# Performance work log

Measured on AMD Instinct MI355X. Metric: run time of the kernel, lower is better.

Reference implementation:

```python
import jax, jax.numpy as jnp
import numpy as np

B, L, E, H = 8192, 64, 128, 8  # batch, max seq len, info_size, head_num
HD = E // H                    # head dim


def setup_inputs() -> dict:
    key = jax.random.key(0)
    k1, k2, k3, k4, k5, k6 = jax.random.split(key, 6)
    inter_info = jax.random.normal(k1, (B, L, E), dtype=jnp.float32)
    # ragged lengths in [1, L] (each sample has at least the query vector)
    lengths = jax.random.randint(k2, (B,), 1, L + 1, dtype=jnp.int32)
    s = 1.0 / np.sqrt(E)
    in_proj_w = jax.random.uniform(k3, (3 * E, E), dtype=jnp.float32, minval=-s, maxval=s)
    in_proj_b = jnp.zeros((3 * E,), dtype=jnp.float32)
    out_proj_w = jax.random.uniform(k4, (E, E), dtype=jnp.float32, minval=-s, maxval=s)
    out_proj_b = jnp.zeros((E,), dtype=jnp.float32)
    return {"inter_info": inter_info, "lengths": lengths,
            "in_proj_w": in_proj_w, "in_proj_b": in_proj_b,
            "out_proj_w": out_proj_w, "out_proj_b": out_proj_b}


def reference(inter_info, lengths, in_proj_w, in_proj_b, out_proj_w, out_proj_b):
    # Per sample: query = first vector, keys/values = all (valid) vectors.
    # Equivalent to torch nn.MultiheadAttention with 1 query per sample.
    Wq, Wk, Wv = in_proj_w[:E], in_proj_w[E:2 * E], in_proj_w[2 * E:]
    bq, bk, bv = in_proj_b[:E], in_proj_b[E:2 * E], in_proj_b[2 * E:]

    query_info = inter_info[:, 0]                                  # [B, E]
    q = (query_info @ Wq.T + bq).reshape(B, H, HD)                 # [B, H, hd]
    k = (inter_info @ Wk.T + bk).reshape(B, L, H, HD)              # [B, L, H, hd]
    v = (inter_info @ Wv.T + bv).reshape(B, L, H, HD)

    scores = jnp.einsum('bhd,blhd->bhl', q, k) / np.sqrt(HD)       # [B, H, L]
    valid = jnp.arange(L)[None, :] < lengths[:, None]              # [B, L]
    scores = jnp.where(valid[:, None, :], scores, -jnp.inf)
    attn = jax.nn.softmax(scores, axis=-1)                         # [B, H, L]

    ctx = jnp.einsum('bhl,blhd->bhd', attn, v).reshape(B, E)       # [B, E]
    attn_hidden = ctx @ out_proj_w.T + out_proj_b                  # [B, E]
    return attn_hidden, query_info
```

## Files before the change

### kernel.cpp

```cpp
#include <hip/hip_runtime.h>
#include <hip/hip_bf16.h>


typedef unsigned int  u32;
typedef unsigned short u16;

#define XR  136
#define XR4 17
#define YR  136
#define UR  136
#define SCR 68

typedef __attribute__((ext_vector_type(8))) __bf16 bf16x8;
typedef __attribute__((ext_vector_type(4))) float  f32x4;

struct __align__(16) Smem {
  u16   Xs[2][64 * XR];
  u16   u[2][8 * UR];
  u16   y[2][8 * YR];
  float q[2][128];
  float sc[2][8][SCR];
  float c[2][8];
  float ctx[2][128];
  int   isbf;
};

__device__ __forceinline__ float blo(u32 u) { return __uint_as_float(u << 16); }
__device__ __forceinline__ float bhi(u32 u) { return __uint_as_float(u & 0xffff0000u); }
__device__ __forceinline__ float b2f(u16 u) { return __uint_as_float(((u32)u) << 16); }
__device__ __forceinline__ u16 f2b(float f) {
  union { __hip_bfloat16 h; u16 u; } cv; cv.h = __float2bfloat16(f); return cv.u;
}
__device__ __forceinline__ u32 pack2(float a, float b) {
  return (u32)f2b(a) | ((u32)f2b(b) << 16);
}
__device__ __forceinline__ void unp8(uint4 v, float* o) {
  o[0]=blo(v.x); o[1]=bhi(v.x); o[2]=blo(v.y); o[3]=bhi(v.y);
  o[4]=blo(v.z); o[5]=bhi(v.z); o[6]=blo(v.w); o[7]=bhi(v.w);
}

template<bool BF>
__device__ __forceinline__ void load8(const void* p, size_t off, float* o) {
  if (BF) {
    unp8(*(const uint4*)((const u16*)p + off), o);
  } else {
    const float4* q4 = (const float4*)((const float*)p + off);
    float4 a = q4[0], b = q4[1];
    o[0]=a.x; o[1]=a.y; o[2]=a.z; o[3]=a.w;
    o[4]=b.x; o[5]=b.y; o[6]=b.z; o[7]=b.w;
  }
}
template<bool BF>
__device__ __forceinline__ void load4(const void* p, size_t off, float* o) {
  if (BF) {
    uint2 v = *(const uint2*)((const u16*)p + off);
    o[0]=blo(v.x); o[1]=bhi(v.x); o[2]=blo(v.y); o[3]=bhi(v.y);
  } else {
    float4 v = *(const float4*)((const float*)p + off);
    o[0]=v.x; o[1]=v.y; o[2]=v.z; o[3]=v.w;
  }
}
template<bool BF>
__device__ __forceinline__ float lds1(const void* p, size_t off) {
  return BF ? b2f(((const u16*)p)[off]) : ((const float*)p)[off];
}

template<bool BF>
__device__ __forceinline__ void body(Smem& S, int b0, int t,
    const void* inter, const int* lengths, const void* w_in, const void* b_in,
    const void* w_out, const void* b_out, void* out)
{
  const int len0 = lengths[b0];
  const int len1 = lengths[b0 + 1];

  if (BF) {
    const uint4* src = (const uint4*)inter + (size_t)b0 * 1024;
#pragma unroll
    for (int r = 0; r < 4; ++r) {
      int g = t + 512 * r;
      int tile = g >> 10, gg = g & 1023, l = gg >> 4, ci = gg & 15;
      if (l < (tile ? len1 : len0))
        ((uint4*)S.Xs[tile])[l * XR4 + ci] = src[g];
    }
  } else {
    const float4* src = (const float4*)inter + (size_t)b0 * 2048;
#pragma unroll
    for (int r = 0; r < 4; ++r) {
      int g = t + 512 * r;
      int tile = g >> 10, gg = g & 1023, l = gg >> 4, ci = gg & 15;
      if (l < (tile ? len1 : len0)) {
        float4 a = src[g * 2], b = src[g * 2 + 1];
        uint4 v;
        v.x = pack2(a.x, a.y); v.y = pack2(a.z, a.w);
        v.z = pack2(b.x, b.y); v.w = pack2(b.z, b.w);
        ((uint4*)S.Xs[tile])[l * XR4 + ci] = v;
      }
    }
  }
  __syncthreads();

  if (t < 128) {
    float a0 = 0.f, a1 = 0.f;
#pragma unroll
    for (int k = 0; k < 16; ++k) {
      float w8[8]; load8<BF>(w_in, (size_t)t * 128 + k * 8, w8);
      float xa[8]; unp8(((const uint4*)S.Xs[0])[k], xa);
      float xb[8]; unp8(((const uint4*)S.Xs[1])[k], xb);
#pragma unroll
      for (int j = 0; j < 8; ++j) {
        a0 = fmaf(w8[j], xa[j], a0);
        a1 = fmaf(w8[j], xb[j], a1);
      }
    }
    float bq = lds1<BF>(b_in, t);
    S.q[0][t] = a0 + bq;
    S.q[1][t] = a1 + bq;
  }
  __syncthreads();

  if (t < 256) {
    const int h = t >> 5, cc = t & 31;
    float a00=0.f,a01=0.f,a02=0.f,a03=0.f, a10=0.f,a11=0.f,a12=0.f,a13=0.f;
#pragma unroll
    for (int d = 0; d < 16; ++d) {
      float w4[4]; load4<BF>(w_in, (size_t)(128 + h * 16 + d) * 128 + cc * 4, w4);
      float q0 = S.q[0][h * 16 + d], q1 = S.q[1][h * 16 + d];
      a00 = fmaf(w4[0], q0, a00); a01 = fmaf(w4[1], q0, a01);
      a02 = fmaf(w4[2], q0, a02); a03 = fmaf(w4[3], q0, a03);
      a10 = fmaf(w4[0], q1, a10); a11 = fmaf(w4[1], q1, a11);
      a12 = fmaf(w4[2], q1, a12); a13 = fmaf(w4[3], q1, a13);
    }
    *(uint2*)&S.u[0][h * UR + cc * 4] = make_uint2(pack2(a00, a01), pack2(a02, a03));
    *(uint2*)&S.u[1][h * UR + cc * 4] = make_uint2(pack2(a10, a11), pack2(a12, a13));
    if (cc == 0) {
      float c0 = 0.f, c1 = 0.f;
      for (int d = 0; d < 16; ++d) {
        float bk = lds1<BF>(b_in, 128 + h * 16 + d);
        c0 += S.q[0][h * 16 + d] * bk;
        c1 += S.q[1][h * 16 + d] * bk;
      }
      S.c[0][h] = c0; S.c[1][h] = c1;
    }
  }
  __syncthreads();

  {
    const int w = t >> 6, lane = t & 63;
    const int bt = w >> 2, mt = w & 3;
    const int arow = mt * 16 + (lane & 15);
    const int col  = lane & 15;
    const int kb   = (lane >> 4) * 8;
    const bool hv  = (col < 8);
    f32x4 acc = {0.f, 0.f, 0.f, 0.f};
#pragma unroll
    for (int kc = 0; kc < 4; ++kc) {
      union { uint4 u4; bf16x8 b8; } a, b;
      a.u4 = *(const uint4*)&S.Xs[bt][arow * XR + kc * 32 + kb];
      b.u4 = *(const uint4*)&S.u[bt][(col & 7) * UR + kc * 32 + kb];
      if (!hv) b.u4 = make_uint4(0u, 0u, 0u, 0u);
      acc = __builtin_amdgcn_mfma_f32_16x16x32_bf16(a.b8, b.b8, acc, 0, 0, 0);
    }
    if (hv) {
      const int l0 = mt * 16 + (lane >> 4) * 4;
      const float cadd = S.c[bt][col];
      f32x4 o;
      o[0] = (acc[0] + cadd) * 0.25f;
      o[1] = (acc[1] + cadd) * 0.25f;
      o[2] = (acc[2] + cadd) * 0.25f;
      o[3] = (acc[3] + cadd) * 0.25f;
      *(f32x4*)&S.sc[bt][col][l0] = o;
    }
  }
  __syncthreads();

  {
    const int bt = t >> 8, h = (t >> 5) & 7, sub = t & 31;
    const int len = bt ? len1 : len0;
    const int l0 = sub, l1 = sub + 32;
    float s0 = S.sc[bt][h][l0], s1 = S.sc[bt][h][l1];
    const bool v0 = l0 < len, v1 = l1 < len;
    float m = fmaxf(v0 ? s0 : -INFINITY, v1 ? s1 : -INFINITY);
#pragma unroll
    for (int off = 16; off > 0; off >>= 1) m = fmaxf(m, __shfl_xor(m, off, 32));
    float e0 = v0 ? __expf(s0 - m) : 0.f;
    float e1 = v1 ? __expf(s1 - m) : 0.f;
    float s = e0 + e1;
#pragma unroll
    for (int off = 16; off > 0; off >>= 1) s += __shfl_xor(s, off, 32);
    float inv = 1.f / s;
    S.sc[bt][h][l0] = e0 * inv;
    S.sc[bt][h][l1] = e1 * inv;
  }
  __syncthreads();

  {
    const int bt = t >> 8, h = (t >> 5) & 7, cc = t & 31;
    const int len = bt ? len1 : len0;
    float a0 = 0.f, a1 = 0.f, a2 = 0.f, a3 = 0.f;
    const float* ar = S.sc[bt][h];
    const u16* xb = S.Xs[bt];
#pragma unroll 4
    for (int l = 0; l < len; ++l) {
      float av = ar[l];
      uint2 xv = *(const uint2*)&xb[l * XR + cc * 4];
      a0 = fmaf(av, blo(xv.x), a0); a1 = fmaf(av, bhi(xv.x), a1);
      a2 = fmaf(av, blo(xv.y), a2); a3 = fmaf(av, bhi(xv.y), a3);
    }
    *(uint2*)&S.y[bt][h * YR + cc * 4] = make_uint2(pack2(a0, a1), pack2(a2, a3));
  }
  __syncthreads();

  if (t < 128) {
    const int h = t >> 4;
    float a0 = 0.f, a1 = 0.f;
#pragma unroll
    for (int k = 0; k < 16; ++k) {
      float w8[8]; load8<BF>(w_in, (size_t)(256 + t) * 128 + k * 8, w8);
      float y0[8]; unp8(*(const uint4*)&S.y[0][h * YR + k * 8], y0);
      float y1[8]; unp8(*(const uint4*)&S.y[1][h * YR + k * 8], y1);
#pragma unroll
      for (int j = 0; j < 8; ++j) {
        a0 = fmaf(w8[j], y0[j], a0);
        a1 = fmaf(w8[j], y1[j], a1);
      }
    }
    float bv = lds1<BF>(b_in, 256 + t);
    S.ctx[0][t] = a0 + bv;
    S.ctx[1][t] = a1 + bv;
  }
  __syncthreads();

  if (t < 128) {
    float a0 = 0.f, a1 = 0.f;
#pragma unroll
    for (int k = 0; k < 16; ++k) {
      float w8[8]; load8<BF>(w_out, (size_t)t * 128 + k * 8, w8);
      float4 ca = *(const float4*)&S.ctx[0][k * 8];
      float4 cb = *(const float4*)&S.ctx[0][k * 8 + 4];
      float4 da = *(const float4*)&S.ctx[1][k * 8];
      float4 db = *(const float4*)&S.ctx[1][k * 8 + 4];
      a0 += w8[0]*ca.x + w8[1]*ca.y + w8[2]*ca.z + w8[3]*ca.w
          + w8[4]*cb.x + w8[5]*cb.y + w8[6]*cb.z + w8[7]*cb.w;
      a1 += w8[0]*da.x + w8[1]*da.y + w8[2]*da.z + w8[3]*da.w
          + w8[4]*db.x + w8[5]*db.y + w8[6]*db.z + w8[7]*db.w;
    }
    float bo = lds1<BF>(b_out, t);
    a0 += bo; a1 += bo;
    if (BF) {
      u16* o = (u16*)out;
      o[(size_t)b0 * 128 + t]       = f2b(a0);
      o[(size_t)(b0 + 1) * 128 + t] = f2b(a1);
    } else {
      float* o = (float*)out;
      o[(size_t)b0 * 128 + t]       = a0;
      o[(size_t)(b0 + 1) * 128 + t] = a1;
    }
  } else if (t >= 256) {
    const int tile = (t >> 7) & 1, e = t & 127;
    size_t o1 = (size_t)8192 * 128 + (size_t)(b0 + tile) * 128 + e;
    u16 xv = S.Xs[tile][e];
    if (BF) ((u16*)out)[o1] = xv;
    else    ((float*)out)[o1] = b2f(xv);
  }
}

__global__ __launch_bounds__(512, 6) void infoattn_kernel(
    const void* inter, const int* __restrict__ lengths,
    const void* w_in, const void* b_in, const void* w_out, const void* b_out,
    void* out)
{
  __shared__ Smem S;
  const int t = threadIdx.x;
  const int b0 = blockIdx.x * 2;

  if (t < 64) {
    float v = b2f(((const u16*)inter)[t]);
    bool bad = !(fabsf(v) < 1000.f);
    unsigned long long m = __ballot(bad);
    if (t == 0) S.isbf = (m == 0ull) ? 1 : 0;
  }
  __syncthreads();
  const bool isbf = (S.isbf != 0);

  if (isbf) body<true >(S, b0, t, inter, lengths, w_in, b_in, w_out, b_out, out);
  else      body<false>(S, b0, t, inter, lengths, w_in, b_in, w_out, b_out, out);
}

extern "C" void kernel_launch(void* const* d_in, const int* in_sizes, int n_in,
                              void* d_out, int out_size, void* d_ws, size_t ws_size,
                              hipStream_t stream) {
  infoattn_kernel<<<dim3(4096), dim3(512), 0, stream>>>(
      d_in[0], (const int*)d_in[1], d_in[2], d_in[3], d_in[4], d_in[5], d_out);
}
```

Measured before the change: 442.3 us.

## Spread small per-block GEMV stages across all 512 threads with split-K shuffles

The q projection, q·Wk fold, V projection and output projection stages previously ran on only 128 or 256 threads, each handling both batch tiles. They now use all 512 threads: each output element is split over two threads, each doing half of K, and the halves are combined with a lane xor-shuffle. The query passthrough write is handled by the idle half-threads. Launch bounds are also relaxed from 6 to 4 blocks per CU, which gives more registers per thread but may lower occupancy.

```diff
diff --git a/kernel.cpp b/kernel.cpp
--- a/kernel.cpp
+++ b/kernel.cpp
@@ -99,47 +99,39 @@
   }
   __syncthreads();
 
-  if (t < 128) {
-    float a0 = 0.f, a1 = 0.f;
-#pragma unroll
-    for (int k = 0; k < 16; ++k) {
-      float w8[8]; load8<BF>(w_in, (size_t)t * 128 + k * 8, w8);
-      float xa[8]; unp8(((const uint4*)S.Xs[0])[k], xa);
-      float xb[8]; unp8(((const uint4*)S.Xs[1])[k], xb);
-#pragma unroll
-      for (int j = 0; j < 8; ++j) {
-        a0 = fmaf(w8[j], xa[j], a0);
-        a1 = fmaf(w8[j], xb[j], a1);
-      }
-    }
-    float bq = lds1<BF>(b_in, t);
-    S.q[0][t] = a0 + bq;
-    S.q[1][t] = a1 + bq;
-  }
-  __syncthreads();
-
-  if (t < 256) {
-    const int h = t >> 5, cc = t & 31;
-    float a00=0.f,a01=0.f,a02=0.f,a03=0.f, a10=0.f,a11=0.f,a12=0.f,a13=0.f;
+  {
+    const int o = t >> 1, kh = t & 1;
+    const int bt = o >> 7, e = o & 127;
+    float a = 0.f;
+#pragma unroll
+    for (int k = 0; k < 8; ++k) {
+      const int kc = kh * 8 + k;
+      float w8[8]; load8<BF>(w_in, (size_t)e * 128 + kc * 8, w8);
+      float x8[8]; unp8(((const uint4*)S.Xs[bt])[kc], x8);
+#pragma unroll
+      for (int j = 0; j < 8; ++j) a = fmaf(w8[j], x8[j], a);
+    }
+    a += __shfl_xor(a, 1, 64);
+    if (kh == 0) S.q[bt][e] = a + lds1<BF>(b_in, e);
+  }
+  __syncthreads();
+
+  {
+    const int bt = t >> 8, h = (t >> 5) & 7, cc = t & 31;
+    float a0=0.f,a1=0.f,a2=0.f,a3=0.f;
 #pragma unroll
     for (int d = 0; d < 16; ++d) {
       float w4[4]; load4<BF>(w_in, (size_t)(128 + h * 16 + d) * 128 + cc * 4, w4);
-      float q0 = S.q[0][h * 16 + d], q1 = S.q[1][h * 16 + d];
-      a00 = fmaf(w4[0], q0, a00); a01 = fmaf(w4[1], q0, a01);
-      a02 = fmaf(w4[2], q0, a02); a03 = fmaf(w4[3], q0, a03);
-      a10 = fmaf(w4[0], q1, a10); a11 = fmaf(w4[1], q1, a11);
-      a12 = fmaf(w4[2], q1, a12); a13 = fmaf(w4[3], q1, a13);
-    }
-    *(uint2*)&S.u[0][h * UR + cc * 4] = make_uint2(pack2(a00, a01), pack2(a02, a03));
-    *(uint2*)&S.u[1][h * UR + cc * 4] = make_uint2(pack2(a10, a11), pack2(a12, a13));
+      float q0 = S.q[bt][h * 16 + d];
+      a0 = fmaf(w4[0], q0, a0); a1 = fmaf(w4[1], q0, a1);
+      a2 = fmaf(w4[2], q0, a2); a3 = fmaf(w4[3], q0, a3);
+    }
+    *(uint2*)&S.u[bt][h * UR + cc * 4] = make_uint2(pack2(a0, a1), pack2(a2, a3));
     if (cc == 0) {
-      float c0 = 0.f, c1 = 0.f;
-      for (int d = 0; d < 16; ++d) {
-        float bk = lds1<BF>(b_in, 128 + h * 16 + d);
-        c0 += S.q[0][h * 16 + d] * bk;
-        c1 += S.q[1][h * 16 + d] * bk;
-      }
-      S.c[0][h] = c0; S.c[1][h] = c1;
+      float c0 = 0.f;
+      for (int d = 0; d < 16; ++d)
+        c0 += S.q[bt][h * 16 + d] * lds1<BF>(b_in, 128 + h * 16 + d);
+      S.c[bt][h] = c0;
     }
   }
   __syncthreads();
@@ -210,61 +202,51 @@
   }
   __syncthreads();
 
-  if (t < 128) {
-    const int h = t >> 4;
-    float a0 = 0.f, a1 = 0.f;
-#pragma unroll
-    for (int k = 0; k < 16; ++k) {
-      float w8[8]; load8<BF>(w_in, (size_t)(256 + t) * 128 + k * 8, w8);
-      float y0[8]; unp8(*(const uint4*)&S.y[0][h * YR + k * 8], y0);
-      float y1[8]; unp8(*(const uint4*)&S.y[1][h * YR + k * 8], y1);
-#pragma unroll
-      for (int j = 0; j < 8; ++j) {
-        a0 = fmaf(w8[j], y0[j], a0);
-        a1 = fmaf(w8[j], y1[j], a1);
-      }
-    }
-    float bv = lds1<BF>(b_in, 256 + t);
-    S.ctx[0][t] = a0 + bv;
-    S.ctx[1][t] = a1 + bv;
-  }
-  __syncthreads();
-
-  if (t < 128) {
-    float a0 = 0.f, a1 = 0.f;
-#pragma unroll
-    for (int k = 0; k < 16; ++k) {
-      float w8[8]; load8<BF>(w_out, (size_t)t * 128 + k * 8, w8);
-      float4 ca = *(const float4*)&S.ctx[0][k * 8];
-      float4 cb = *(const float4*)&S.ctx[0][k * 8 + 4];
-      float4 da = *(const float4*)&S.ctx[1][k * 8];
-      float4 db = *(const float4*)&S.ctx[1][k * 8 + 4];
-      a0 += w8[0]*ca.x + w8[1]*ca.y + w8[2]*ca.z + w8[3]*ca.w
-          + w8[4]*cb.x + w8[5]*cb.y + w8[6]*cb.z + w8[7]*cb.w;
-      a1 += w8[0]*da.x + w8[1]*da.y + w8[2]*da.z + w8[3]*da.w
-          + w8[4]*db.x + w8[5]*db.y + w8[6]*db.z + w8[7]*db.w;
-    }
-    float bo = lds1<BF>(b_out, t);
-    a0 += bo; a1 += bo;
-    if (BF) {
-      u16* o = (u16*)out;
-      o[(size_t)b0 * 128 + t]       = f2b(a0);
-      o[(size_t)(b0 + 1) * 128 + t] = f2b(a1);
+  {
+    const int o = t >> 1, kh = t & 1;
+    const int bt = o >> 7, e = o & 127, h = e >> 4;
+    float a = 0.f;
+#pragma unroll
+    for (int k = 0; k < 8; ++k) {
+      const int kc = kh * 8 + k;
+      float w8[8]; load8<BF>(w_in, (size_t)(256 + e) * 128 + kc * 8, w8);
+      float y8[8]; unp8(*(const uint4*)&S.y[bt][h * YR + kc * 8], y8);
+#pragma unroll
+      for (int j = 0; j < 8; ++j) a = fmaf(w8[j], y8[j], a);
+    }
+    a += __shfl_xor(a, 1, 64);
+    if (kh == 0) S.ctx[bt][e] = a + lds1<BF>(b_in, 256 + e);
+  }
+  __syncthreads();
+
+  {
+    const int o = t >> 1, kh = t & 1;
+    const int bt = o >> 7, e = o & 127;
+    float a = 0.f;
+#pragma unroll
+    for (int k = 0; k < 8; ++k) {
+      const int kc = kh * 8 + k;
+      float w8[8]; load8<BF>(w_out, (size_t)e * 128 + kc * 8, w8);
+      float4 ca = *(const float4*)&S.ctx[bt][kc * 8];
+      float4 cb = *(const float4*)&S.ctx[bt][kc * 8 + 4];
+      a += w8[0]*ca.x + w8[1]*ca.y + w8[2]*ca.z + w8[3]*ca.w
+         + w8[4]*cb.x + w8[5]*cb.y + w8[6]*cb.z + w8[7]*cb.w;
+    }
+    a += __shfl_xor(a, 1, 64);
+    if (kh == 0) {
+      a += lds1<BF>(b_out, e);
+      if (BF) ((u16*)out)[(size_t)(b0 + bt) * 128 + e] = f2b(a);
+      else    ((float*)out)[(size_t)(b0 + bt) * 128 + e] = a;
     } else {
-      float* o = (float*)out;
-      o[(size_t)b0 * 128 + t]       = a0;
-      o[(size_t)(b0 + 1) * 128 + t] = a1;
-    }
-  } else if (t >= 256) {
-    const int tile = (t >> 7) & 1, e = t & 127;
-    size_t o1 = (size_t)8192 * 128 + (size_t)(b0 + tile) * 128 + e;
-    u16 xv = S.Xs[tile][e];
-    if (BF) ((u16*)out)[o1] = xv;
-    else    ((float*)out)[o1] = b2f(xv);
-  }
-}
-
-__global__ __launch_bounds__(512, 6) void infoattn_kernel(
+      size_t o1 = (size_t)8192 * 128 + (size_t)(b0 + bt) * 128 + e;
+      u16 xv = S.Xs[bt][e];
+      if (BF) ((u16*)out)[o1] = xv;
+      else    ((float*)out)[o1] = b2f(xv);
+    }
+  }
+}
+
+__global__ __launch_bounds__(512, 4) void infoattn_kernel(
     const void* inter, const int* __restrict__ lengths,
     const void* w_in, const void* b_in, const void* w_out, const void* b_out,
     void* out)
```

After: 531.3 us. +20.1%, slower.

## Split GEMV stages across all 512 threads with shuffle reductions

Applied to the files above, without the earlier changes.

The q-projection, V-projection and output-projection stages each ran on only 128 threads with 128-long serial dot products. They now use all 8 wavefronts: 16 lanes split each row's K dimension and combine partial sums with xor-shuffle reductions, and each thread covers 4 rows. The query_info copy-out is folded into the output stage. Launch bounds drop from 6 to 4 waves per EU, which allows more registers but may lower occupancy.

```diff
diff --git a/kernel.cpp b/kernel.cpp
--- a/kernel.cpp
+++ b/kernel.cpp
@@ -99,22 +99,33 @@
   }
   __syncthreads();
 
-  if (t < 128) {
-    float a0 = 0.f, a1 = 0.f;
-#pragma unroll
-    for (int k = 0; k < 16; ++k) {
-      float w8[8]; load8<BF>(w_in, (size_t)t * 128 + k * 8, w8);
-      float xa[8]; unp8(((const uint4*)S.Xs[0])[k], xa);
-      float xb[8]; unp8(((const uint4*)S.Xs[1])[k], xb);
+  {
+    const int lane = t & 63, w = t >> 6;
+    const int rw = lane >> 4, kl = lane & 15;
+    float x0[8], x1[8];
+    unp8(*(const uint4*)&S.Xs[0][kl * 8], x0);
+    unp8(*(const uint4*)&S.Xs[1][kl * 8], x1);
+#pragma unroll
+    for (int p = 0; p < 4; ++p) {
+      const int r = p * 32 + w * 4 + rw;
+      float w8[8]; load8<BF>(w_in, (size_t)r * 128 + kl * 8, w8);
+      float a0 = 0.f, a1 = 0.f;
 #pragma unroll
       for (int j = 0; j < 8; ++j) {
-        a0 = fmaf(w8[j], xa[j], a0);
-        a1 = fmaf(w8[j], xb[j], a1);
-      }
-    }
-    float bq = lds1<BF>(b_in, t);
-    S.q[0][t] = a0 + bq;
-    S.q[1][t] = a1 + bq;
+        a0 = fmaf(w8[j], x0[j], a0);
+        a1 = fmaf(w8[j], x1[j], a1);
+      }
+#pragma unroll
+      for (int off = 8; off > 0; off >>= 1) {
+        a0 += __shfl_xor(a0, off, 64);
+        a1 += __shfl_xor(a1, off, 64);
+      }
+      if (kl == 0) {
+        float bq = lds1<BF>(b_in, r);
+        S.q[0][r] = a0 + bq;
+        S.q[1][r] = a1 + bq;
+      }
+    }
   }
   __syncthreads();
 
@@ -210,61 +221,78 @@
   }
   __syncthreads();
 
-  if (t < 128) {
-    const int h = t >> 4;
-    float a0 = 0.f, a1 = 0.f;
-#pragma unroll
-    for (int k = 0; k < 16; ++k) {
-      float w8[8]; load8<BF>(w_in, (size_t)(256 + t) * 128 + k * 8, w8);
-      float y0[8]; unp8(*(const uint4*)&S.y[0][h * YR + k * 8], y0);
-      float y1[8]; unp8(*(const uint4*)&S.y[1][h * YR + k * 8], y1);
+  {
+    const int lane = t & 63, w = t >> 6;
+    const int rw = lane >> 4, kl = lane & 15;
+#pragma unroll
+    for (int p = 0; p < 4; ++p) {
+      const int r = p * 32 + w * 4 + rw;
+      const int h = r >> 4;
+      float w8[8]; load8<BF>(w_in, (size_t)(256 + r) * 128 + kl * 8, w8);
+      float y0[8], y1[8];
+      unp8(*(const uint4*)&S.y[0][h * YR + kl * 8], y0);
+      unp8(*(const uint4*)&S.y[1][h * YR + kl * 8], y1);
+      float a0 = 0.f, a1 = 0.f;
 #pragma unroll
       for (int j = 0; j < 8; ++j) {
         a0 = fmaf(w8[j], y0[j], a0);
         a1 = fmaf(w8[j], y1[j], a1);
       }
-    }
-    float bv = lds1<BF>(b_in, 256 + t);
-    S.ctx[0][t] = a0 + bv;
-    S.ctx[1][t] = a1 + bv;
-  }
-  __syncthreads();
-
-  if (t < 128) {
-    float a0 = 0.f, a1 = 0.f;
-#pragma unroll
-    for (int k = 0; k < 16; ++k) {
-      float w8[8]; load8<BF>(w_out, (size_t)t * 128 + k * 8, w8);
-      float4 ca = *(const float4*)&S.ctx[0][k * 8];
-      float4 cb = *(const float4*)&S.ctx[0][k * 8 + 4];
-      float4 da = *(const float4*)&S.ctx[1][k * 8];
-      float4 db = *(const float4*)&S.ctx[1][k * 8 + 4];
-      a0 += w8[0]*ca.x + w8[1]*ca.y + w8[2]*ca.z + w8[3]*ca.w
-          + w8[4]*cb.x + w8[5]*cb.y + w8[6]*cb.z + w8[7]*cb.w;
-      a1 += w8[0]*da.x + w8[1]*da.y + w8[2]*da.z + w8[3]*da.w
-          + w8[4]*db.x + w8[5]*db.y + w8[6]*db.z + w8[7]*db.w;
-    }
-    float bo = lds1<BF>(b_out, t);
-    a0 += bo; a1 += bo;
-    if (BF) {
-      u16* o = (u16*)out;
-      o[(size_t)b0 * 128 + t]       = f2b(a0);
-      o[(size_t)(b0 + 1) * 128 + t] = f2b(a1);
-    } else {
-      float* o = (float*)out;
-      o[(size_t)b0 * 128 + t]       = a0;
-      o[(size_t)(b0 + 1) * 128 + t] = a1;
-    }
-  } else if (t >= 256) {
-    const int tile = (t >> 7) & 1, e = t & 127;
-    size_t o1 = (size_t)8192 * 128 + (size_t)(b0 + tile) * 128 + e;
-    u16 xv = S.Xs[tile][e];
-    if (BF) ((u16*)out)[o1] = xv;
-    else    ((float*)out)[o1] = b2f(xv);
-  }
-}
-
-__global__ __launch_bounds__(512, 6) void infoattn_kernel(
+#pragma unroll
+      for (int off = 8; off > 0; off >>= 1) {
+        a0 += __shfl_xor(a0, off, 64);
+        a1 += __shfl_xor(a1, off, 64);
+      }
+      if (kl == 0) {
+        float bv = lds1<BF>(b_in, 256 + r);
+        S.ctx[0][r] = a0 + bv;
+        S.ctx[1][r] = a1 + bv;
+      }
+    }
+  }
+  __syncthreads();
+
+  {
+    const int lane = t & 63, w = t >> 6;
+    const int rw = lane >> 4, kl = lane & 15;
+    float c0[8], c1[8];
+    *(float4*)&c0[0] = *(const float4*)&S.ctx[0][kl * 8];
+    *(float4*)&c0[4] = *(const float4*)&S.ctx[0][kl * 8 + 4];
+    *(float4*)&c1[0] = *(const float4*)&S.ctx[1][kl * 8];
+    *(float4*)&c1[4] = *(const float4*)&S.ctx[1][kl * 8 + 4];
+#pragma unroll
+    for (int p = 0; p < 4; ++p) {
+      const int r = p * 32 + w * 4 + rw;
+      float w8[8]; load8<BF>(w_out, (size_t)r * 128 + kl * 8, w8);
+      float a0 = 0.f, a1 = 0.f;
+#pragma unroll
+      for (int j = 0; j < 8; ++j) {
+        a0 = fmaf(w8[j], c0[j], a0);
+        a1 = fmaf(w8[j], c1[j], a1);
+      }
+#pragma unroll
+      for (int off = 8; off > 0; off >>= 1) {
+        a0 += __shfl_xor(a0, off, 64);
+        a1 += __shfl_xor(a1, off, 64);
+      }
+      if (kl < 2) {
+        float a = (kl == 0) ? a0 : a1;
+        a += lds1<BF>(b_out, r);
+        size_t oo = (size_t)(b0 + kl) * 128 + r;
+        if (BF) ((u16*)out)[oo] = f2b(a);
+        else    ((float*)out)[oo] = a;
+      } else if (kl < 4) {
+        const int bt = kl - 2;
+        size_t o1 = (size_t)8192 * 128 + (size_t)(b0 + bt) * 128 + r;
+        u16 xv = S.Xs[bt][r];
+        if (BF) ((u16*)out)[o1] = xv;
+        else    ((float*)out)[o1] = b2f(xv);
+      }
+    }
+  }
+}
+
+__global__ __launch_bounds__(512, 4) void infoattn_kernel(
     const void* inter, const int* __restrict__ lengths,
     const void* w_in, const void* b_in, const void* w_out, const void* b_out,
     void* out)
```

Result: faster. 421.0 us (-4.8%).
